# Performance work log

Hardware: AMD Instinct MI355X
Metric: run time of the kernel (lower is better)

The kernel has to match this reference:

```python
import jax, jax.numpy as jnp
import numpy as np

B, G, L, S = 4096, 16000, 64, 20000  # batch spots, genes, labels, total spots
LOG_2PI = float(np.log(2.0 * np.pi))


def _log_nb_positive_altparam(x, r, o):
    # NB with total_count r > 0 and logits o (stereoscope parametrization)
    return (jax.lax.lgamma(x + r) - jax.lax.lgamma(r) - jax.lax.lgamma(x + 1.0)
            + x * jax.nn.log_sigmoid(o) + r * jax.nn.log_sigmoid(-o))


def setup_inputs() -> dict:
    key = jax.random.key(0)
    ks = jax.random.split(key, 8)
    x = jax.random.randint(ks[0], (B, G), 0, 100, dtype=jnp.int32)
    y = jax.random.randint(ks[1], (B, 1), 0, L, dtype=jnp.int32)
    ind_x = jax.random.randint(ks[2], (B, 1), 0, S, dtype=jnp.int32)
    W = jax.random.normal(ks[3], (G, L), dtype=jnp.float32)          # fixed dictionary
    px_o = 0.5 * jax.random.normal(ks[4], (G,), dtype=jnp.float32)   # fixed log-odds
    eta = jax.random.normal(ks[5], (G,), dtype=jnp.float32)
    V = jax.random.normal(ks[6], (L + 1, S), dtype=jnp.float32)
    beta = 0.1 * jax.random.normal(ks[7], (G,), dtype=jnp.float32)
    return {"x": x, "y": y, "ind_x": ind_x, "W": W, "px_o": px_o,
            "eta": eta, "V": V, "beta": beta}


def reference(x, y, ind_x, W, px_o, eta, V, beta):
    x_f = x.astype(jnp.float32)                      # [B, G]
    beta_sp = jax.nn.softplus(beta)                  # [G]
    w_sp = jax.nn.softplus(W)                        # [G, L]
    eps_sp = jax.nn.softplus(eta)                    # [G]
    # r_hat = [beta*W | eps]  -> [G, L+1]
    r_hat = jnp.concatenate([beta_sp[:, None] * w_sp, eps_sp[:, None]], axis=1)
    # column-gather from V (embedding lookup over spots), then softplus
    v_ind = jax.nn.softplus(V[:, ind_x[:, 0]])       # [L+1, B]
    # thin matmul, inner dim L+1; px_rate: [B, G]
    px_rate = jnp.einsum("gl,lb->bg", r_hat, v_ind)
    # NB reconstruction loss per spot
    reconst_loss = -jnp.sum(_log_nb_positive_altparam(x_f, px_rate, px_o[None, :]), axis=-1)  # [B]
    # -sum log N(eta; 0, 1)
    neg_log_likelihood_prior = jnp.sum(0.5 * LOG_2PI + 0.5 * eta * eta)
    return (reconst_loss, jnp.float32(0.0), neg_log_likelihood_prior)
```

## Files before the change

### kernel.cpp

```cpp
#include <hip/hip_runtime.h>
#include <hip/hip_bf16.h>
#include <math.h>

#define Gn 16000
#define Bn 4096
#define Ln 64
#define Sn 20000
#define NGT 250
#define GENE_BLOCKS 4000
#define SPOT_BLOCKS 1024

typedef __attribute__((ext_vector_type(8))) short bf16x8;
typedef __attribute__((ext_vector_type(4))) float f32x4;


__device__ __forceinline__ float softplus_precise(float z) {
    return fmaxf(z, 0.0f) + log1pf(__expf(-fabsf(z)));
}

__device__ __forceinline__ float lgamma_pos8(float z) {
    float p = z * (z + 1.f) * (z + 2.f) * (z + 3.f)
                * (z + 4.f) * (z + 5.f) * (z + 6.f) * (z + 7.f);
    float w = z + 8.f;
    return (w - 0.5f) * __logf(w) - w + 0.9189385332046727f
           + __fdividef(1.0f, 12.0f * w) - __logf(p);
}

__device__ __forceinline__ unsigned short f2bf(float f) {
    union { float f; unsigned int u; } v; v.f = f;
    unsigned int r = v.u + 0x7fff + ((v.u >> 16) & 1);
    return (unsigned short)(r >> 16);
}


__global__ void prep_fused(const float* __restrict__ W,
                           const float* __restrict__ px_o,
                           const float* __restrict__ eta,
                           const float* __restrict__ beta,
                           const float* __restrict__ V,
                           const int*   __restrict__ ind_x,
                           unsigned short* __restrict__ rhB,
                           float* __restrict__ lsp1,
                           float* __restrict__ lsn,
                           float* __restrict__ eps,
                           unsigned short* __restrict__ vBg,
                           float* __restrict__ v64,
                           float* __restrict__ prior_part) {
    const int bid = blockIdx.x;
    const int tid = threadIdx.x;
    if (bid < GENE_BLOCKS) {
        int idx = bid * 256 + tid;
        int g = idx >> 6;
        float bsp = softplus_precise(beta[g]);
        rhB[idx] = f2bf(bsp * softplus_precise(W[idx]));
        float s = 0.f;
        if (idx < Gn) {
            eps[idx] = softplus_precise(eta[idx]);
            float o = px_o[idx];
            lsp1[idx] = -softplus_precise(-o) - 1.0f;
            lsn[idx]  = -softplus_precise(o);
            float e = eta[idx];
            s = 0.9189385332046727f + 0.5f * e * e;
        }
        if (bid < 64) {
            #pragma unroll
            for (int off = 32; off; off >>= 1) s += __shfl_xor(s, off, 64);
            __shared__ float red[4];
            if ((tid & 63) == 0) red[tid >> 6] = s;
            __syncthreads();
            if (tid == 0) prior_part[bid] = red[0] + red[1] + red[2] + red[3];
        }
    } else {
        int idx = (bid - GENE_BLOCKS) * 256 + tid;
        int b = idx >> 6, l = idx & 63;
        int s = ind_x[b];
        vBg[idx] = f2bf(softplus_precise(V[l * Sn + s]));
        if (idx < Bn) {
            int s2 = ind_x[idx];
            v64[idx] = softplus_precise(V[Ln * Sn + s2]);
        }
    }
}


__global__ __launch_bounds__(256) void main_kernel(
    const int*            __restrict__ x,
    const unsigned short* __restrict__ rhB,
    const unsigned short* __restrict__ vBg,
    const float*          __restrict__ v64,
    const float*          __restrict__ lsp1g,
    const float*          __restrict__ lsng,
    const float*          __restrict__ epsg,
    float*                __restrict__ partial) {
    __shared__ __align__(16) unsigned short sA[64][72];
    __shared__ __align__(16) unsigned short sB[64][72];
    __shared__ float sv64[64];
    __shared__ float sLsp1[64], sLsn[64], sEps[64];
    __shared__ float lfact[100];
    __shared__ float pred[64];

    const int tid = threadIdx.x;
    const int g0 = blockIdx.x * 64;
    const int b0 = blockIdx.y * 64;

    {
        int row = tid >> 3;
        int c   = (tid & 7) * 8;
        *(uint4*)&sA[row][c]      = *(const uint4*)&vBg[(b0 + row) * 64 + c];
        *(uint4*)&sA[row + 32][c] = *(const uint4*)&vBg[(b0 + row + 32) * 64 + c];
        *(uint4*)&sB[row][c]      = *(const uint4*)&rhB[(g0 + row) * 64 + c];
        *(uint4*)&sB[row + 32][c] = *(const uint4*)&rhB[(g0 + row + 32) * 64 + c];
    }
    if (tid < 64) {
        sv64[tid]  = v64[b0 + tid];
        sLsp1[tid] = lsp1g[g0 + tid];
        sLsn[tid]  = lsng[g0 + tid];
        sEps[tid]  = epsg[g0 + tid];
    }
    if (tid < 100) lfact[tid] = lgamma_pos8((float)tid + 1.0f);

    const int wave = tid >> 6, lane = tid & 63;
    const int quad = lane >> 4, ln = lane & 15;
    const int mrow  = wave * 16 + ln;
    const int brow0 = b0 + wave * 16 + quad * 4;

    int xv[4][4];
    #pragma unroll
    for (int nb = 0; nb < 4; nb++) {
        int g = g0 + nb * 16 + ln;
        #pragma unroll
        for (int r = 0; r < 4; r++)
            xv[nb][r] = x[(size_t)(brow0 + r) * Gn + g];
    }

    f32x4 acc[4];
    #pragma unroll
    for (int nb = 0; nb < 4; nb++) acc[nb] = (f32x4){0.f, 0.f, 0.f, 0.f};

    __syncthreads();

    #pragma unroll
    for (int kb = 0; kb < 2; kb++) {
        bf16x8 af = *(const bf16x8*)&sA[mrow][kb * 32 + quad * 8];
        #pragma unroll
        for (int nb = 0; nb < 4; nb++) {
            bf16x8 bfr = *(const bf16x8*)&sB[nb * 16 + ln][kb * 32 + quad * 8];
            acc[nb] = __builtin_amdgcn_mfma_f32_16x16x32_bf16(af, bfr, acc[nb], 0, 0, 0);
        }
    }

    float vvr[4];
    #pragma unroll
    for (int r = 0; r < 4; r++) vvr[r] = sv64[wave * 16 + quad * 4 + r];

    float rowpart[4] = {0.f, 0.f, 0.f, 0.f};
    #pragma unroll
    for (int nb = 0; nb < 4; nb++) {
        const float lsp1v = sLsp1[nb * 16 + ln];
        const float lsnv  = sLsn[nb * 16 + ln];
        const float ev    = sEps[nb * 16 + ln];
        #pragma unroll
        for (int r = 0; r < 4; r++) {
            const float rr = fmaf(ev, vvr[r], acc[nb][r]);
            const int   xi = xv[nb][r];
            const float xf = (float)xi;
            const float s  = rr + xf;
            float t = fmaf(s - 0.5f, __logf(s), -lfact[xi]);
            t = fmaf(-(rr - 0.5f), __logf(rr), t);
            t = fmaf(xf, lsp1v, t);
            t = fmaf(rr, lsnv, t);
            rowpart[r] += t;
        }
    }

    #pragma unroll
    for (int r = 0; r < 4; r++) {
        float v = rowpart[r];
        v += __shfl_xor(v, 1, 64);
        v += __shfl_xor(v, 2, 64);
        v += __shfl_xor(v, 4, 64);
        v += __shfl_xor(v, 8, 64);
        if (ln == 0) pred[wave * 16 + quad * 4 + r] = v;
    }
    __syncthreads();
    if (tid < 64) partial[(size_t)blockIdx.x * Bn + b0 + tid] = pred[tid];
}

__global__ __launch_bounds__(256) void reduce_kernel(const float* __restrict__ partial,
                                                     const float* __restrict__ prior_part,
                                                     float* __restrict__ out) {
    int b = blockIdx.x * 256 + threadIdx.x;
    float s0 = 0.f, s1 = 0.f, s2 = 0.f, s3 = 0.f, s4 = 0.f;
    for (int i = 0; i < NGT; i += 5) {
        s0 += partial[(size_t)(i + 0) * Bn + b];
        s1 += partial[(size_t)(i + 1) * Bn + b];
        s2 += partial[(size_t)(i + 2) * Bn + b];
        s3 += partial[(size_t)(i + 3) * Bn + b];
        s4 += partial[(size_t)(i + 4) * Bn + b];
    }
    out[b] = -(s0 + s1 + s2 + s3 + s4);

    if (blockIdx.x == 0) {
        int tid = threadIdx.x;
        if (tid < 64) {
            float s = prior_part[tid];
            #pragma unroll
            for (int off = 32; off; off >>= 1) s += __shfl_xor(s, off, 64);
            if (tid == 0) {
                out[Bn]     = 0.0f;
                out[Bn + 1] = s;
            }
        }
    }
}


extern "C" void kernel_launch(void* const* d_in, const int* in_sizes, int n_in,
                              void* d_out, int out_size, void* d_ws, size_t ws_size,
                              hipStream_t stream) {
    const int*   x     = (const int*)d_in[0];
    const int*   ind_x = (const int*)d_in[2];
    const float* W     = (const float*)d_in[3];
    const float* px_o  = (const float*)d_in[4];
    const float* eta   = (const float*)d_in[5];
    const float* V     = (const float*)d_in[6];
    const float* beta  = (const float*)d_in[7];
    float* out = (float*)d_out;

    char* wsb = (char*)d_ws;
    unsigned short* rhB   = (unsigned short*)(wsb);
    unsigned short* vBg   = (unsigned short*)(wsb + 2048000);
    float*          v64   = (float*)(wsb + 2572288);
    float*          lsp1  = (float*)(wsb + 2588672);
    float*          lsn   = (float*)(wsb + 2652672);
    float*          eps   = (float*)(wsb + 2716672);
    float*          part  = (float*)(wsb + 2780672);
    float*          prio  = (float*)(wsb + 6876672);

    prep_fused<<<GENE_BLOCKS + SPOT_BLOCKS, 256, 0, stream>>>(
        W, px_o, eta, beta, V, ind_x, rhB, lsp1, lsn, eps, vBg, v64, prio);

    dim3 grid(Gn / 64, Bn / 64);
    main_kernel<<<grid, 256, 0, stream>>>(x, rhB, vBg, v64, lsp1, lsn, eps, part);

    reduce_kernel<<<Bn / 256, 256, 0, stream>>>(part, prio, out);
}
```

Before: 391.2 us.

## Retile main kernel to 16-spot by 320-gene tiles with coalesced x staging

Changes the main kernel tile from 64x64 (spots x genes) to 16 spots x 320 genes. Each block stages its x tile through LDS with vectorized int4 loads. Each wave keeps its A fragment in registers and reads rhB straight from global memory, which shrinks the partial-sum buffer and the reduce work by a factor of five. The aim is to replace the strided scalar x reads with coalesced wide loads and to cut partial-sum traffic. In exchange, rhB is re-read from global for every 16-spot tile, and the per-gene parameter loads lose reuse.

```diff
diff --git a/kernel.cpp b/kernel.cpp
--- a/kernel.cpp
+++ b/kernel.cpp
@@ -6,7 +6,10 @@
 #define Bn 4096
 #define Ln 64
 #define Sn 20000
-#define NGT 250
+#define GT 320
+#define NGT 50
+#define BT 16
+#define XP 324
 #define GENE_BLOCKS 4000
 #define SPOT_BLOCKS 1024
 
@@ -83,7 +86,7 @@
 }
 
 
-__global__ __launch_bounds__(256) void main_kernel(
+__global__ __launch_bounds__(256, 4) void main_kernel(
     const int*            __restrict__ x,
     const unsigned short* __restrict__ rhB,
     const unsigned short* __restrict__ vBg,
@@ -92,98 +95,79 @@
     const float*          __restrict__ lsng,
     const float*          __restrict__ epsg,
     float*                __restrict__ partial) {
-    __shared__ __align__(16) unsigned short sA[64][72];
-    __shared__ __align__(16) unsigned short sB[64][72];
-    __shared__ float sv64[64];
-    __shared__ float sLsp1[64], sLsn[64], sEps[64];
+    __shared__ __align__(16) int sX[BT * XP];
     __shared__ float lfact[100];
-    __shared__ float pred[64];
-
-    const int tid = threadIdx.x;
-    const int g0 = blockIdx.x * 64;
-    const int b0 = blockIdx.y * 64;
-
-    {
-        int row = tid >> 3;
-        int c   = (tid & 7) * 8;
-        *(uint4*)&sA[row][c]      = *(const uint4*)&vBg[(b0 + row) * 64 + c];
-        *(uint4*)&sA[row + 32][c] = *(const uint4*)&vBg[(b0 + row + 32) * 64 + c];
-        *(uint4*)&sB[row][c]      = *(const uint4*)&rhB[(g0 + row) * 64 + c];
-        *(uint4*)&sB[row + 32][c] = *(const uint4*)&rhB[(g0 + row + 32) * 64 + c];
-    }
-    if (tid < 64) {
-        sv64[tid]  = v64[b0 + tid];
-        sLsp1[tid] = lsp1g[g0 + tid];
-        sLsn[tid]  = lsng[g0 + tid];
-        sEps[tid]  = epsg[g0 + tid];
-    }
-    if (tid < 100) lfact[tid] = lgamma_pos8((float)tid + 1.0f);
-
+    __shared__ float pred[4][16];
+
+    const int tid  = threadIdx.x;
     const int wave = tid >> 6, lane = tid & 63;
     const int quad = lane >> 4, ln = lane & 15;
-    const int mrow  = wave * 16 + ln;
-    const int brow0 = b0 + wave * 16 + quad * 4;
-
-    int xv[4][4];
+    const int gt = blockIdx.x;
+    const int b0 = blockIdx.y * BT;
+    const int g0 = gt * GT;
+
     #pragma unroll
-    for (int nb = 0; nb < 4; nb++) {
-        int g = g0 + nb * 16 + ln;
+    for (int i = 0; i < 5; ++i) {
+        int F   = i * 256 + tid;
+        int row = F / 80;
+        int c4  = F - row * 80;
+        int4 v = *(const int4*)&x[(size_t)(b0 + row) * Gn + g0 + c4 * 4];
+        *(int4*)&sX[row * XP + c4 * 4] = v;
+    }
+
+    bf16x8 av0 = *(const bf16x8*)&vBg[(b0 + ln) * 64 + quad * 8];
+    bf16x8 av1 = *(const bf16x8*)&vBg[(b0 + ln) * 64 + 32 + quad * 8];
+    float4 vv4 = *(const float4*)&v64[b0 + quad * 4];
+    float vvr[4] = {vv4.x, vv4.y, vv4.z, vv4.w};
+
+    if (tid < 100) lfact[tid] = lgamma_pos8((float)tid + 1.0f);
+
+    __syncthreads();
+
+    float rowacc[4] = {0.f, 0.f, 0.f, 0.f};
+    #pragma unroll
+    for (int nb = 0; nb < 5; ++nb) {
+        const int gl = wave * 80 + nb * 16 + ln;
+        const int gg = g0 + gl;
+        const unsigned short* rrow = &rhB[(size_t)gg * 64];
+        bf16x8 bf0 = *(const bf16x8*)&rrow[quad * 8];
+        bf16x8 bf1 = *(const bf16x8*)&rrow[32 + quad * 8];
+        f32x4 a = (f32x4){0.f, 0.f, 0.f, 0.f};
+        a = __builtin_amdgcn_mfma_f32_16x16x32_bf16(av0, bf0, a, 0, 0, 0);
+        a = __builtin_amdgcn_mfma_f32_16x16x32_bf16(av1, bf1, a, 0, 0, 0);
+
+        const float lsp1v = lsp1g[gg];
+        const float lsnv  = lsng[gg];
+        const float ev    = epsg[gg];
         #pragma unroll
-        for (int r = 0; r < 4; r++)
-            xv[nb][r] = x[(size_t)(brow0 + r) * Gn + g];
-    }
-
-    f32x4 acc[4];
-    #pragma unroll
-    for (int nb = 0; nb < 4; nb++) acc[nb] = (f32x4){0.f, 0.f, 0.f, 0.f};
-
-    __syncthreads();
-
-    #pragma unroll
-    for (int kb = 0; kb < 2; kb++) {
-        bf16x8 af = *(const bf16x8*)&sA[mrow][kb * 32 + quad * 8];
-        #pragma unroll
-        for (int nb = 0; nb < 4; nb++) {
-            bf16x8 bfr = *(const bf16x8*)&sB[nb * 16 + ln][kb * 32 + quad * 8];
-            acc[nb] = __builtin_amdgcn_mfma_f32_16x16x32_bf16(af, bfr, acc[nb], 0, 0, 0);
-        }
-    }
-
-    float vvr[4];
-    #pragma unroll
-    for (int r = 0; r < 4; r++) vvr[r] = sv64[wave * 16 + quad * 4 + r];
-
-    float rowpart[4] = {0.f, 0.f, 0.f, 0.f};
-    #pragma unroll
-    for (int nb = 0; nb < 4; nb++) {
-        const float lsp1v = sLsp1[nb * 16 + ln];
-        const float lsnv  = sLsn[nb * 16 + ln];
-        const float ev    = sEps[nb * 16 + ln];
-        #pragma unroll
-        for (int r = 0; r < 4; r++) {
-            const float rr = fmaf(ev, vvr[r], acc[nb][r]);
-            const int   xi = xv[nb][r];
+        for (int r = 0; r < 4; ++r) {
+            const int row = quad * 4 + r;
+            const int xi  = sX[row * XP + gl];
+            const float rr = fmaf(ev, vvr[r], a[r]);
             const float xf = (float)xi;
             const float s  = rr + xf;
-            float t = fmaf(s - 0.5f, __logf(s), -lfact[xi]);
-            t = fmaf(-(rr - 0.5f), __logf(rr), t);
-            t = fmaf(xf, lsp1v, t);
-            t = fmaf(rr, lsnv, t);
-            rowpart[r] += t;
+            float tt = fmaf(s - 0.5f, __logf(s), -lfact[xi]);
+            tt = fmaf(-(rr - 0.5f), __logf(rr), tt);
+            tt = fmaf(xf, lsp1v, tt);
+            tt = fmaf(rr, lsnv, tt);
+            rowacc[r] += tt;
         }
     }
 
     #pragma unroll
-    for (int r = 0; r < 4; r++) {
-        float v = rowpart[r];
+    for (int r = 0; r < 4; ++r) {
+        float v = rowacc[r];
         v += __shfl_xor(v, 1, 64);
         v += __shfl_xor(v, 2, 64);
         v += __shfl_xor(v, 4, 64);
         v += __shfl_xor(v, 8, 64);
-        if (ln == 0) pred[wave * 16 + quad * 4 + r] = v;
+        if (ln == 0) pred[wave][quad * 4 + r] = v;
     }
     __syncthreads();
-    if (tid < 64) partial[(size_t)blockIdx.x * Bn + b0 + tid] = pred[tid];
+    if (tid < BT) {
+        float s = pred[0][tid] + pred[1][tid] + pred[2][tid] + pred[3][tid];
+        partial[(size_t)gt * Bn + b0 + tid] = s;
+    }
 }
 
 __global__ __launch_bounds__(256) void reduce_kernel(const float* __restrict__ partial,
@@ -235,12 +219,12 @@
     float*          lsn   = (float*)(wsb + 2652672);
     float*          eps   = (float*)(wsb + 2716672);
     float*          part  = (float*)(wsb + 2780672);
-    float*          prio  = (float*)(wsb + 6876672);
+    float*          prio  = (float*)(wsb + 3599872);
 
     prep_fused<<<GENE_BLOCKS + SPOT_BLOCKS, 256, 0, stream>>>(
         W, px_o, eta, beta, V, ind_x, rhB, lsp1, lsn, eps, vBg, v64, prio);
 
-    dim3 grid(Gn / 64, Bn / 64);
+    dim3 grid(NGT, Bn / BT);
     main_kernel<<<grid, 256, 0, stream>>>(x, rhB, vBg, v64, lsp1, lsn, eps, part);
 
     reduce_kernel<<<Bn / 256, 256, 0, stream>>>(part, prio, out);
```

After: 395.6 us. Within noise of the previous version (+1.1%).
